# Kernel tuning notes

Hardware: AMD Instinct MI355X
Metric: run time of the kernel (lower is better)

The kernel has to match this reference:

```python
import jax, jax.numpy as jnp
import numpy as np

EMBED = 1024
ATTN = 1024
HEADS = 16
HEAD_DIM = ATTN // HEADS


def setup_inputs() -> dict:
    key = jax.random.key(0)
    ks = jax.random.split(key, 8)
    s = 1.0 / np.sqrt(EMBED)
    sa = 1.0 / np.sqrt(ATTN)
    return {
        "queries": jax.random.normal(ks[0], (4, 512, EMBED), jnp.float32),
        "context": jax.random.normal(ks[1], (4, 2048, EMBED), jnp.float32),
        "Wq": jax.random.normal(ks[2], (EMBED, ATTN), jnp.float32) * s,
        "bq": jnp.zeros((ATTN,), jnp.float32),
        "Wkv": jax.random.normal(ks[3], (EMBED, 2 * ATTN), jnp.float32) * s,
        "bkv": jnp.zeros((2 * ATTN,), jnp.float32),
        "Wo": jax.random.normal(ks[4], (ATTN, EMBED), jnp.float32) * sa,
        "bo": jnp.zeros((EMBED,), jnp.float32),
    }


def reference(queries, context, Wq, bq, Wkv, bkv, Wo, bo):
    B, Lq, _ = queries.shape
    Lk = context.shape[1]
    q = queries @ Wq + bq                      # [B, Lq, ATTN]
    kv = context @ Wkv + bkv                   # [B, Lk, 2*ATTN]
    k, v = jnp.split(kv, 2, axis=-1)
    q = q.reshape(B, Lq, HEADS, HEAD_DIM)
    k = k.reshape(B, Lk, HEADS, HEAD_DIM)
    v = v.reshape(B, Lk, HEADS, HEAD_DIM)
    scale = 1.0 / np.sqrt(HEAD_DIM)
    scores = jnp.einsum("bqhd,bkhd->bhqk", q, k) * scale
    attn = jax.nn.softmax(scores, axis=-1)
    x = jnp.einsum("bhqk,bkhd->bqhd", attn, v).reshape(B, Lq, ATTN)
    return x @ Wo + bo
```

## Files before the change

### kernel.cpp

```cpp
#include <hip/hip_runtime.h>
#include <hip/hip_bf16.h>
#include <stdint.h>

typedef unsigned short u16;
typedef __attribute__((ext_vector_type(8))) __bf16 bf16x8;
typedef __attribute__((ext_vector_type(2))) __bf16 bf16x2;
typedef __attribute__((ext_vector_type(4))) float f32x4;
typedef __attribute__((ext_vector_type(4))) u16 u16x4;
typedef __attribute__((ext_vector_type(4))) float f32x4v;

typedef __attribute__((address_space(1))) void gvoid_t;
typedef __attribute__((address_space(3))) void lvoid_t;

#define BAR()    asm volatile("s_barrier" ::: "memory")
#define WAITV0() asm volatile("s_waitcnt vmcnt(0)" ::: "memory")
#define WAITV2() asm volatile("s_waitcnt vmcnt(2)" ::: "memory")
#define WAITV4() asm volatile("s_waitcnt vmcnt(4)" ::: "memory")
#define WAITV8() asm volatile("s_waitcnt vmcnt(8)" ::: "memory")

__device__ inline u16 f2bf(float f) {
    uint32_t u = __float_as_uint(f);
    u += 0x7fff + ((u >> 16) & 1);
    return (u16)(u >> 16);
}

__device__ inline float bf2f(u16 v) {
    return __uint_as_float(((uint32_t)v) << 16);
}

__device__ inline void gll16(const void* g, void* l) {
    __builtin_amdgcn_global_load_lds((gvoid_t*)g, (lvoid_t*)l, 16, 0, 0);
}

__device__ inline f32x4 mfma16(bf16x8 a, bf16x8 b, f32x4 c) {
    return __builtin_amdgcn_mfma_f32_16x16x32_bf16(a, b, c, 0, 0, 0);
}

__device__ inline int vslot(int r) {
    int n = r >> 4;
    return ((n >> 1) << 5) + (((r >> 2) & 3) << 3) + ((n & 1) << 2) + (r & 3);
}

__global__ __launch_bounds__(256) void cast_bf16_kernel(
        const float* __restrict__ in, u16* __restrict__ out, int n4) {
    int i = blockIdx.x * 256 + threadIdx.x;
    if (i >= n4) return;
    f32x4v f = ((const f32x4v*)in)[i];
    u16x4 o;
    o[0] = f2bf(f[0]); o[1] = f2bf(f[1]); o[2] = f2bf(f[2]); o[3] = f2bf(f[3]);
    ((u16x4*)out)[i] = o;
}

__global__ __launch_bounds__(256) void trans_cast_kernel(
        const float* __restrict__ W, u16* __restrict__ WT, int K, int N) {
    __shared__ float t[32][33];
    int x = threadIdx.x;
    int y = threadIdx.y;
    int n0 = blockIdx.x * 32;
    int k0 = blockIdx.y * 32;
    for (int yy = y; yy < 32; yy += 8)
        t[yy][x] = W[(size_t)(k0 + yy) * N + n0 + x];
    __syncthreads();
    for (int yy = y; yy < 32; yy += 8)
        WT[(size_t)(n0 + yy) * K + k0 + x] = f2bf(t[x][yy]);
}

template <int MODE>
__global__ __launch_bounds__(512, 2) void gemm_bt(
        const u16* __restrict__ A, const u16* __restrict__ Bt,
        const float* __restrict__ bias, int M, int N, int K,
        float scale, void* __restrict__ out0) {
    __shared__ u16 lds[4][2][128 * 32];
    const int NT = K >> 5;
    const int tid = threadIdx.x;
    const int lane = tid & 63, wv = tid >> 6;
    const int c16 = lane & 15, g = lane >> 4;
    const int m0 = blockIdx.y * 128, n0 = blockIdx.x * 128;

    const int r0 = tid >> 2, cc0 = (tid & 3) ^ ((r0 >> 1) & 3);
    const size_t offA = (size_t)(m0 + r0) * K + cc0 * 8;
    const size_t offB = (size_t)(n0 + r0) * K + cc0 * 8;
    const int dstw = wv * 512;

    auto stage = [&](int t) {
        gll16(A + offA + t * 32, &lds[t & 3][0][0] + dstw);
        gll16(Bt + offB + t * 32, &lds[t & 3][1][0] + dstw);
    };

    const int wm = (wv >> 1) * 32, wn = (wv & 1) * 64;
    f32x4 acc[2][4] = {};

    auto compute = [&](int slot) {
        const u16* la = &lds[slot][0][0];
        const u16* lb = &lds[slot][1][0];
        bf16x8 af[2], bfr[4];
#pragma unroll
        for (int m = 0; m < 2; m++) {
            int row = wm + m * 16 + c16;
            af[m] = *(const bf16x8*)&la[row * 32 + (g ^ ((row >> 1) & 3)) * 8];
        }
#pragma unroll
        for (int n = 0; n < 4; n++) {
            int row = wn + n * 16 + c16;
            bfr[n] = *(const bf16x8*)&lb[row * 32 + (g ^ ((row >> 1) & 3)) * 8];
        }
#pragma unroll
        for (int m = 0; m < 2; m++)
#pragma unroll
            for (int n = 0; n < 4; n++)
                acc[m][n] = mfma16(af[m], bfr[n], acc[m][n]);
    };

    stage(0); stage(1); stage(2);

    for (int t = 0; t < NT - 2; ++t) {
        WAITV4();
        BAR();
        if (t + 3 < NT) stage(t + 3);
        compute(t & 3);
    }
    WAITV2(); BAR(); compute((NT - 2) & 3);
    WAITV0(); BAR(); compute((NT - 1) & 3);

#pragma unroll
    for (int n = 0; n < 4; n++) {
        int col = n0 + wn + n * 16 + c16;
        float bv = bias[col];
#pragma unroll
        for (int m = 0; m < 2; m++) {
            int rowb = m0 + wm + m * 16 + g * 4;
#pragma unroll
            for (int j = 0; j < 4; j++) {
                float v = (acc[m][n][j] + bv) * scale;
                int row = rowb + j;
                if (MODE == 0) {
                    ((u16*)out0)[(size_t)row * N + col] = f2bf(v);
                } else {
                    ((float*)out0)[(size_t)row * N + col] = v;
                }
            }
        }
    }
}

__global__ __launch_bounds__(512, 2) void gemm_kv_ring(
        const u16* __restrict__ A, const u16* __restrict__ Bt,
        const float* __restrict__ bias, u16* __restrict__ Kp,
        u16* __restrict__ VpT) {
    __shared__ u16 lds[4][2][256 * 32];
    const int K = 1024, NT = 32;
    const int tid = threadIdx.x;
    const int lane = tid & 63, wv = tid >> 6;
    const int c16 = lane & 15, g = lane >> 4;

    const int nwg = gridDim.x * gridDim.y;
    const int bid = blockIdx.y * gridDim.x + blockIdx.x;
    const int cpx = nwg >> 3;
    const int sw = (bid & 7) * cpx + (bid >> 3);
    const int bx = sw % gridDim.x, by = sw / gridDim.x;
    const int m0 = by * 256, n0 = bx * 256;

    const int isB = wv >> 2;
    const int rbase = (wv & 3) * 64;
    const u16* src = isB ? Bt : A;
    const int base0 = isB ? n0 : m0;
    size_t off[4];
    const u16* ldst[4];
#pragma unroll
    for (int i = 0; i < 4; i++) {
        int rl = rbase + i * 16 + (lane >> 2);
        int ch = (lane & 3) ^ ((rl >> 1) & 3);
        off[i] = (size_t)(base0 + rl) * K + ch * 8;
        ldst[i] = &lds[0][0][0] + ((size_t)isB * 256 * 32) + (size_t)(rbase + i * 16) * 32;
    }
    const size_t slotStride = 2 * 256 * 32;

    auto stage = [&](int t) {
        const u16* s0 = src + (size_t)t * 32;
        u16* d = (u16*)ldst[0] + (size_t)(t & 3) * slotStride;
        gll16(s0 + off[0], d);
        gll16(s0 + off[1], d + 16 * 32);
        gll16(s0 + off[2], d + 32 * 32);
        gll16(s0 + off[3], d + 48 * 32);
    };

    const int wm = wv >> 2;
    const int wn = wv & 3;
    f32x4 acc[8][4] = {};

    auto compute = [&](int slot) {
        const u16* la = &lds[slot][0][0];
        const u16* lb = &lds[slot][1][0];
        bf16x8 af[8], bfr[4];
#pragma unroll
        for (int m = 0; m < 8; m++) {
            int row = wm * 128 + m * 16 + c16;
            af[m] = *(const bf16x8*)&la[row * 32 + (g ^ ((row >> 1) & 3)) * 8];
        }
#pragma unroll
        for (int n = 0; n < 4; n++) {
            int row = wn * 64 + n * 16 + c16;
            bfr[n] = *(const bf16x8*)&lb[row * 32 + (g ^ ((row >> 1) & 3)) * 8];
        }
#pragma unroll
        for (int m = 0; m < 8; m++)
#pragma unroll
            for (int n = 0; n < 4; n++)
                acc[m][n] = mfma16(af[m], bfr[n], acc[m][n]);
    };

    stage(0); stage(1); stage(2);

    for (int t = 0; t < NT - 2; ++t) {
        WAITV8();
        BAR();
        if (t + 3 < NT) stage(t + 3);
        compute(t & 3);
    }
    WAITV4(); BAR(); compute((NT - 2) & 3);
    WAITV0(); BAR(); compute((NT - 1) & 3);

    const bool isV = (n0 >= 1024);
#pragma unroll
    for (int n = 0; n < 4; n++) {
        int col = n0 + wn * 64 + n * 16 + c16;
        float bv = bias[col];
#pragma unroll
        for (int m = 0; m < 8; m++) {
            int rowb = m0 + wm * 128 + m * 16 + g * 4;
            if (isV) {
                u16x4 pk;
#pragma unroll
                for (int j = 0; j < 4; j++) pk[j] = f2bf(acc[m][n][j] + bv);
                int vcol = (rowb & ~63) + vslot(rowb & 63);
                *(u16x4*)&VpT[(size_t)(col - 1024) * 8192 + vcol] = pk;
            } else {
#pragma unroll
                for (int j = 0; j < 4; j++)
                    Kp[(size_t)(rowb + j) * 1024 + col] = f2bf(acc[m][n][j] + bv);
            }
        }
    }
}

__global__ __launch_bounds__(512, 4) void attn_split_kernel(
        const u16* __restrict__ Qp, const u16* __restrict__ Kp,
        const u16* __restrict__ VpT, u16* __restrict__ Opart,
        float* __restrict__ ml) {
    __shared__ u16 lKV[3][2][64 * 64];
    const int NT = 16;
    const int tid = threadIdx.x;
    const int lane = tid & 63, wv = tid >> 6;
    const int c16 = lane & 15, g = lane >> 4;
    const int bid = blockIdx.x;
    const int qblk = bid >> 7;
    const int low = bid & 127;
    const int h = low & 15, z = low >> 4;
    const int b = z >> 1, sp = z & 1;
    const int kvbase = sp * 1024;

    const int qrow = b * 512 + qblk * 128 + wv * 16 + c16;
    bf16x8 qf[2];
    qf[0] = *(const bf16x8*)(Qp + (size_t)qrow * 1024 + h * 64 + g * 8);
    qf[1] = *(const bf16x8*)(Qp + (size_t)qrow * 1024 + h * 64 + 32 + g * 8);

    f32x4 acc[4] = {};
    float m_s = -1e30f, l_s = 0.f;

    const int r0 = tid >> 3, c0 = (tid & 7) ^ (r0 & 7);
    const int dstw = wv * 512;

    auto stageKV = [&](int t) {
        int slot = t % 3;
        int kv0 = kvbase + t * 64;
        u16* dK = &lKV[slot][0][0];
        u16* dV = &lKV[slot][1][0];
        gll16(Kp + (size_t)(b * 2048 + kv0 + r0) * 1024 + h * 64 + c0 * 8, dK + dstw);
        gll16(VpT + (size_t)(h * 64 + r0) * 8192 + b * 2048 + kv0 + c0 * 8, dV + dstw);
    };

    stageKV(0); stageKV(1);
    for (int t = 0; t < NT; ++t) {
        if (t < NT - 2) { WAITV2(); } else { WAITV0(); }
        BAR();
        if (t + 2 < NT) stageKV(t + 2);

        const int slot = t % 3;
        const u16* lK = &lKV[slot][0][0];
        const u16* lV = &lKV[slot][1][0];

        f32x4 s[4];
#pragma unroll
        for (int n = 0; n < 4; n++) {
            s[n] = f32x4{0.f, 0.f, 0.f, 0.f};
            int key = n * 16 + c16;
#pragma unroll
            for (int kk = 0; kk < 2; kk++) {
                bf16x8 kf = *(const bf16x8*)&lK[key * 64 + (((kk * 4 + g) ^ (key & 7))) * 8];
                s[n] = mfma16(kf, qf[kk], s[n]);
            }
        }

        float mn0 = fmaxf(fmaxf(s[0][0], s[0][1]), fmaxf(s[0][2], s[0][3]));
        float mn1 = fmaxf(fmaxf(s[1][0], s[1][1]), fmaxf(s[1][2], s[1][3]));
        float mn2 = fmaxf(fmaxf(s[2][0], s[2][1]), fmaxf(s[2][2], s[2][3]));
        float mn3 = fmaxf(fmaxf(s[3][0], s[3][1]), fmaxf(s[3][2], s[3][3]));
        float mx = fmaxf(fmaxf(mn0, mn1), fmaxf(mn2, mn3));
        mx = fmaxf(mx, __shfl_xor(mx, 16));
        mx = fmaxf(mx, __shfl_xor(mx, 32));

        if (!__all(mx - m_s <= 8.0f)) {
            float mn = fmaxf(m_s, mx);
            float al = exp2f(m_s - mn);
            m_s = mn;
            l_s *= al;
            float alr[4];
#pragma unroll
            for (int j = 0; j < 4; j++) alr[j] = __shfl(al, g * 4 + j);
#pragma unroll
            for (int nd = 0; nd < 4; nd++)
#pragma unroll
                for (int j = 0; j < 4; j++) acc[nd][j] *= alr[j];
        }

        uint32_t r[4][2];
        float sums[4];
#pragma unroll
        for (int n = 0; n < 4; n++) {
            float p0 = exp2f(s[n][0] - m_s);
            float p1 = exp2f(s[n][1] - m_s);
            float p2 = exp2f(s[n][2] - m_s);
            float p3 = exp2f(s[n][3] - m_s);
            sums[n] = (p0 + p1) + (p2 + p3);
            union { bf16x2 h; uint32_t u; } ca, cb;
            ca.h[0] = (__bf16)p0; ca.h[1] = (__bf16)p1;
            cb.h[0] = (__bf16)p2; cb.h[1] = (__bf16)p3;
            r[n][0] = ca.u; r[n][1] = cb.u;
        }
        float sum = (sums[0] + sums[1]) + (sums[2] + sums[3]);
        sum += __shfl_xor(sum, 16);
        sum += __shfl_xor(sum, 32);
        l_s += sum;

#pragma unroll
        for (int kk2 = 0; kk2 < 2; kk2++) {
            union { bf16x8 v8; uint32_t u[4]; } pa;
            pa.u[0] = r[kk2 * 2][0];
            pa.u[1] = r[kk2 * 2][1];
            pa.u[2] = r[kk2 * 2 + 1][0];
            pa.u[3] = r[kk2 * 2 + 1][1];
#pragma unroll
            for (int nd = 0; nd < 4; nd++) {
                int d = nd * 16 + c16;
                bf16x8 vf = *(const bf16x8*)&lV[d * 64 + (((kk2 * 4 + g) ^ (d & 7))) * 8];
                acc[nd] = mfma16(pa.v8, vf, acc[nd]);
            }
        }
    }

#pragma unroll
    for (int j = 0; j < 4; j++) {
        int rowq = b * 512 + qblk * 128 + wv * 16 + g * 4 + j;
        size_t idx = (size_t)sp * 32768 + (size_t)rowq * 16 + h;
#pragma unroll
        for (int nd = 0; nd < 4; nd++)
            Opart[idx * 64 + nd * 16 + c16] = f2bf(acc[nd][j]);
    }
    if (g == 0) {
        int rowq = b * 512 + qblk * 128 + wv * 16 + c16;
        size_t idx = (size_t)sp * 32768 + (size_t)rowq * 16 + h;
        ml[idx * 2] = m_s;
        ml[idx * 2 + 1] = l_s;
    }
}

__global__ __launch_bounds__(256) void attn_combine_kernel(
        const u16* __restrict__ Opart, const float* __restrict__ ml,
        u16* __restrict__ X) {
    const int tid = threadIdx.x;
    const int r = blockIdx.x * 4 + (tid >> 6);
    const int d = tid & 63;
    float m0 = ml[(size_t)r * 2], l0 = ml[(size_t)r * 2 + 1];
    float m1 = ml[(size_t)(32768 + r) * 2], l1 = ml[(size_t)(32768 + r) * 2 + 1];
    float M = fmaxf(m0, m1);
    float a0 = exp2f(m0 - M), a1 = exp2f(m1 - M);
    float li = 1.f / (l0 * a0 + l1 * a1);
    float o0 = bf2f(Opart[(size_t)r * 64 + d]);
    float o1 = bf2f(Opart[(size_t)(32768 + r) * 64 + d]);
    float o = (o0 * a0 + o1 * a1) * li;
    int qrow = r >> 4, h = r & 15;
    X[(size_t)qrow * 1024 + h * 64 + d] = f2bf(o);
}

extern "C" void kernel_launch(void* const* d_in, const int* in_sizes, int n_in,
                              void* d_out, int out_size, void* d_ws, size_t ws_size,
                              hipStream_t stream) {
    const float* queries = (const float*)d_in[0];
    const float* context = (const float*)d_in[1];
    const float* Wq      = (const float*)d_in[2];
    const float* bq      = (const float*)d_in[3];
    const float* Wkv     = (const float*)d_in[4];
    const float* bkv     = (const float*)d_in[5];
    const float* Wo      = (const float*)d_in[6];
    const float* bo      = (const float*)d_in[7];

    char* ws = (char*)d_ws;
    u16* qb   = (u16*)(ws);
    u16* cb   = (u16*)(ws + (4ull  << 20));
    u16* WqT  = (u16*)(ws + (20ull << 20));
    u16* WkvT = (u16*)(ws + (22ull << 20));
    u16* WoT  = (u16*)(ws + (26ull << 20));
    u16* Qp   = (u16*)(ws + (28ull << 20));
    u16* Kp   = (u16*)(ws + (32ull << 20));
    u16* VpT  = (u16*)(ws + (48ull << 20));
    u16* X    = (u16*)(ws + (64ull << 20));
    float* ml    = (float*)qb;
    u16*   Opart = (u16*)cb;

    cast_bf16_kernel<<<dim3(2048), dim3(256), 0, stream>>>(queries, qb, 524288);
    cast_bf16_kernel<<<dim3(8192), dim3(256), 0, stream>>>(context, cb, 2097152);
    trans_cast_kernel<<<dim3(32, 32), dim3(32, 8), 0, stream>>>(Wq, WqT, 1024, 1024);
    trans_cast_kernel<<<dim3(64, 32), dim3(32, 8), 0, stream>>>(Wkv, WkvT, 1024, 2048);
    trans_cast_kernel<<<dim3(32, 32), dim3(32, 8), 0, stream>>>(Wo, WoT, 1024, 1024);

    gemm_bt<0><<<dim3(8, 16), dim3(512), 0, stream>>>(qb, WqT, bq, 2048, 1024, 1024,
                                                      0.18033688f, (void*)Qp);
    gemm_kv_ring<<<dim3(8, 32), dim3(512), 0, stream>>>(cb, WkvT, bkv, Kp, VpT);
    attn_split_kernel<<<dim3(512), dim3(512), 0, stream>>>(Qp, Kp, VpT, Opart, ml);
    attn_combine_kernel<<<dim3(8192), dim3(256), 0, stream>>>(Opart, ml, X);
    gemm_bt<2><<<dim3(8, 16), dim3(512), 0, stream>>>(X, WoT, bo, 2048, 1024, 1024,
                                                      1.0f, d_out);
}
```

Baseline: 131.6 us.

## Process two query subtiles per wave in attention and merge prep kernels

The attention kernel drops to 256 threads per block, and each wave now handles two 16-row query subtiles. Each K/V fragment read from LDS is reused for twice as many MFMAs, and each thread issues four staging loads per tile instead of two. Separately, the two input cast launches are fused into one, and the three weight transpose-cast launches are fused into one 3D grid, cutting launch count. Register pressure in the attention kernel roughly doubles for accumulators and scores, and the wait count changes to vmcnt(4).

```diff
diff --git a/kernel.cpp b/kernel.cpp
--- a/kernel.cpp
+++ b/kernel.cpp
@@ -41,21 +41,32 @@
     return ((n >> 1) << 5) + (((r >> 2) & 3) << 3) + ((n & 1) << 2) + (r & 3);
 }
 
-__global__ __launch_bounds__(256) void cast_bf16_kernel(
-        const float* __restrict__ in, u16* __restrict__ out, int n4) {
+__global__ __launch_bounds__(256) void prep_cast_kernel(
+        const float* __restrict__ q, const float* __restrict__ c,
+        u16* __restrict__ qb, u16* __restrict__ cb) {
     int i = blockIdx.x * 256 + threadIdx.x;
-    if (i >= n4) return;
-    f32x4v f = ((const f32x4v*)in)[i];
+    const float* src; u16* dst; int j;
+    if (i < 524288) { src = q; dst = qb; j = i; }
+    else            { src = c; dst = cb; j = i - 524288; }
+    f32x4v f = ((const f32x4v*)src)[j];
     u16x4 o;
     o[0] = f2bf(f[0]); o[1] = f2bf(f[1]); o[2] = f2bf(f[2]); o[3] = f2bf(f[3]);
-    ((u16x4*)out)[i] = o;
-}
-
-__global__ __launch_bounds__(256) void trans_cast_kernel(
-        const float* __restrict__ W, u16* __restrict__ WT, int K, int N) {
+    ((u16x4*)dst)[j] = o;
+}
+
+__global__ __launch_bounds__(256) void prep_trans_kernel(
+        const float* __restrict__ Wq, const float* __restrict__ Wkv,
+        const float* __restrict__ Wo, u16* __restrict__ WqT,
+        u16* __restrict__ WkvT, u16* __restrict__ WoT) {
+    const int zz = blockIdx.z;
+    const float* W = (zz == 0) ? Wq : (zz == 1) ? Wkv : Wo;
+    u16* WT = (zz == 0) ? WqT : (zz == 1) ? WkvT : WoT;
+    const int N = (zz == 1) ? 2048 : 1024;
+    const int K = 1024;
+    if (blockIdx.x * 32 >= N) return;
     __shared__ float t[32][33];
-    int x = threadIdx.x;
-    int y = threadIdx.y;
+    int x = threadIdx.x & 31;
+    int y = threadIdx.x >> 5;
     int n0 = blockIdx.x * 32;
     int k0 = blockIdx.y * 32;
     for (int yy = y; yy < 32; yy += 8)
@@ -243,7 +254,7 @@
     }
 }
 
-__global__ __launch_bounds__(512, 4) void attn_split_kernel(
+__global__ __launch_bounds__(256, 3) void attn_split_kernel(
         const u16* __restrict__ Qp, const u16* __restrict__ Kp,
         const u16* __restrict__ VpT, u16* __restrict__ Opart,
         float* __restrict__ ml) {
@@ -259,29 +270,35 @@
     const int b = z >> 1, sp = z & 1;
     const int kvbase = sp * 1024;
 
-    const int qrow = b * 512 + qblk * 128 + wv * 16 + c16;
-    bf16x8 qf[2];
-    qf[0] = *(const bf16x8*)(Qp + (size_t)qrow * 1024 + h * 64 + g * 8);
-    qf[1] = *(const bf16x8*)(Qp + (size_t)qrow * 1024 + h * 64 + 32 + g * 8);
-
-    f32x4 acc[4] = {};
-    float m_s = -1e30f, l_s = 0.f;
+    bf16x8 qf[2][2];
+#pragma unroll
+    for (int qs = 0; qs < 2; qs++) {
+        int qrow = b * 512 + qblk * 128 + qs * 64 + wv * 16 + c16;
+        qf[qs][0] = *(const bf16x8*)(Qp + (size_t)qrow * 1024 + h * 64 + g * 8);
+        qf[qs][1] = *(const bf16x8*)(Qp + (size_t)qrow * 1024 + h * 64 + 32 + g * 8);
+    }
+
+    f32x4 acc[2][4] = {};
+    float m_s[2] = {-1e30f, -1e30f}, l_s[2] = {0.f, 0.f};
 
     const int r0 = tid >> 3, c0 = (tid & 7) ^ (r0 & 7);
-    const int dstw = wv * 512;
+    const int r1 = 32 + r0,  c1 = (tid & 7) ^ (r1 & 7);
+    const int dst0 = wv * 512, dst1 = 2048 + wv * 512;
 
     auto stageKV = [&](int t) {
         int slot = t % 3;
         int kv0 = kvbase + t * 64;
         u16* dK = &lKV[slot][0][0];
         u16* dV = &lKV[slot][1][0];
-        gll16(Kp + (size_t)(b * 2048 + kv0 + r0) * 1024 + h * 64 + c0 * 8, dK + dstw);
-        gll16(VpT + (size_t)(h * 64 + r0) * 8192 + b * 2048 + kv0 + c0 * 8, dV + dstw);
+        gll16(Kp + (size_t)(b * 2048 + kv0 + r0) * 1024 + h * 64 + c0 * 8, dK + dst0);
+        gll16(Kp + (size_t)(b * 2048 + kv0 + r1) * 1024 + h * 64 + c1 * 8, dK + dst1);
+        gll16(VpT + (size_t)(h * 64 + r0) * 8192 + b * 2048 + kv0 + c0 * 8, dV + dst0);
+        gll16(VpT + (size_t)(h * 64 + r1) * 8192 + b * 2048 + kv0 + c1 * 8, dV + dst1);
     };
 
     stageKV(0); stageKV(1);
     for (int t = 0; t < NT; ++t) {
-        if (t < NT - 2) { WAITV2(); } else { WAITV0(); }
+        if (t < NT - 1) { WAITV4(); } else { WAITV0(); }
         BAR();
         if (t + 2 < NT) stageKV(t + 2);
 
@@ -289,88 +306,100 @@
         const u16* lK = &lKV[slot][0][0];
         const u16* lV = &lKV[slot][1][0];
 
-        f32x4 s[4];
+        f32x4 s[2][4];
 #pragma unroll
         for (int n = 0; n < 4; n++) {
-            s[n] = f32x4{0.f, 0.f, 0.f, 0.f};
+            s[0][n] = f32x4{0.f, 0.f, 0.f, 0.f};
+            s[1][n] = f32x4{0.f, 0.f, 0.f, 0.f};
+        }
+#pragma unroll
+        for (int n = 0; n < 4; n++) {
             int key = n * 16 + c16;
 #pragma unroll
             for (int kk = 0; kk < 2; kk++) {
                 bf16x8 kf = *(const bf16x8*)&lK[key * 64 + (((kk * 4 + g) ^ (key & 7))) * 8];
-                s[n] = mfma16(kf, qf[kk], s[n]);
-            }
-        }
-
-        float mn0 = fmaxf(fmaxf(s[0][0], s[0][1]), fmaxf(s[0][2], s[0][3]));
-        float mn1 = fmaxf(fmaxf(s[1][0], s[1][1]), fmaxf(s[1][2], s[1][3]));
-        float mn2 = fmaxf(fmaxf(s[2][0], s[2][1]), fmaxf(s[2][2], s[2][3]));
-        float mn3 = fmaxf(fmaxf(s[3][0], s[3][1]), fmaxf(s[3][2], s[3][3]));
-        float mx = fmaxf(fmaxf(mn0, mn1), fmaxf(mn2, mn3));
-        mx = fmaxf(mx, __shfl_xor(mx, 16));
-        mx = fmaxf(mx, __shfl_xor(mx, 32));
-
-        if (!__all(mx - m_s <= 8.0f)) {
-            float mn = fmaxf(m_s, mx);
-            float al = exp2f(m_s - mn);
-            m_s = mn;
-            l_s *= al;
-            float alr[4];
-#pragma unroll
-            for (int j = 0; j < 4; j++) alr[j] = __shfl(al, g * 4 + j);
-#pragma unroll
-            for (int nd = 0; nd < 4; nd++)
-#pragma unroll
-                for (int j = 0; j < 4; j++) acc[nd][j] *= alr[j];
-        }
-
-        uint32_t r[4][2];
-        float sums[4];
-#pragma unroll
-        for (int n = 0; n < 4; n++) {
-            float p0 = exp2f(s[n][0] - m_s);
-            float p1 = exp2f(s[n][1] - m_s);
-            float p2 = exp2f(s[n][2] - m_s);
-            float p3 = exp2f(s[n][3] - m_s);
-            sums[n] = (p0 + p1) + (p2 + p3);
-            union { bf16x2 h; uint32_t u; } ca, cb;
-            ca.h[0] = (__bf16)p0; ca.h[1] = (__bf16)p1;
-            cb.h[0] = (__bf16)p2; cb.h[1] = (__bf16)p3;
-            r[n][0] = ca.u; r[n][1] = cb.u;
-        }
-        float sum = (sums[0] + sums[1]) + (sums[2] + sums[3]);
-        sum += __shfl_xor(sum, 16);
-        sum += __shfl_xor(sum, 32);
-        l_s += sum;
+                s[0][n] = mfma16(kf, qf[0][kk], s[0][n]);
+                s[1][n] = mfma16(kf, qf[1][kk], s[1][n]);
+            }
+        }
+
+        uint32_t r[2][4][2];
+#pragma unroll
+        for (int qs = 0; qs < 2; qs++) {
+            float mn0 = fmaxf(fmaxf(s[qs][0][0], s[qs][0][1]), fmaxf(s[qs][0][2], s[qs][0][3]));
+            float mn1 = fmaxf(fmaxf(s[qs][1][0], s[qs][1][1]), fmaxf(s[qs][1][2], s[qs][1][3]));
+            float mn2 = fmaxf(fmaxf(s[qs][2][0], s[qs][2][1]), fmaxf(s[qs][2][2], s[qs][2][3]));
+            float mn3 = fmaxf(fmaxf(s[qs][3][0], s[qs][3][1]), fmaxf(s[qs][3][2], s[qs][3][3]));
+            float mx = fmaxf(fmaxf(mn0, mn1), fmaxf(mn2, mn3));
+            mx = fmaxf(mx, __shfl_xor(mx, 16));
+            mx = fmaxf(mx, __shfl_xor(mx, 32));
+
+            if (!__all(mx - m_s[qs] <= 8.0f)) {
+                float mn = fmaxf(m_s[qs], mx);
+                float al = exp2f(m_s[qs] - mn);
+                m_s[qs] = mn;
+                l_s[qs] *= al;
+                float alr[4];
+#pragma unroll
+                for (int j = 0; j < 4; j++) alr[j] = __shfl(al, g * 4 + j);
+#pragma unroll
+                for (int nd = 0; nd < 4; nd++)
+#pragma unroll
+                    for (int j = 0; j < 4; j++) acc[qs][nd][j] *= alr[j];
+            }
+
+            float sums[4];
+#pragma unroll
+            for (int n = 0; n < 4; n++) {
+                float p0 = exp2f(s[qs][n][0] - m_s[qs]);
+                float p1 = exp2f(s[qs][n][1] - m_s[qs]);
+                float p2 = exp2f(s[qs][n][2] - m_s[qs]);
+                float p3 = exp2f(s[qs][n][3] - m_s[qs]);
+                sums[n] = (p0 + p1) + (p2 + p3);
+                union { bf16x2 h; uint32_t u; } ca, cb;
+                ca.h[0] = (__bf16)p0; ca.h[1] = (__bf16)p1;
+                cb.h[0] = (__bf16)p2; cb.h[1] = (__bf16)p3;
+                r[qs][n][0] = ca.u; r[qs][n][1] = cb.u;
+            }
+            float sum = (sums[0] + sums[1]) + (sums[2] + sums[3]);
+            sum += __shfl_xor(sum, 16);
+            sum += __shfl_xor(sum, 32);
+            l_s[qs] += sum;
+        }
 
 #pragma unroll
         for (int kk2 = 0; kk2 < 2; kk2++) {
-            union { bf16x8 v8; uint32_t u[4]; } pa;
-            pa.u[0] = r[kk2 * 2][0];
-            pa.u[1] = r[kk2 * 2][1];
-            pa.u[2] = r[kk2 * 2 + 1][0];
-            pa.u[3] = r[kk2 * 2 + 1][1];
+            union { bf16x8 v8; uint32_t u[4]; } pa0, pa1;
+            pa0.u[0] = r[0][kk2 * 2][0];     pa0.u[1] = r[0][kk2 * 2][1];
+            pa0.u[2] = r[0][kk2 * 2 + 1][0]; pa0.u[3] = r[0][kk2 * 2 + 1][1];
+            pa1.u[0] = r[1][kk2 * 2][0];     pa1.u[1] = r[1][kk2 * 2][1];
+            pa1.u[2] = r[1][kk2 * 2 + 1][0]; pa1.u[3] = r[1][kk2 * 2 + 1][1];
 #pragma unroll
             for (int nd = 0; nd < 4; nd++) {
                 int d = nd * 16 + c16;
                 bf16x8 vf = *(const bf16x8*)&lV[d * 64 + (((kk2 * 4 + g) ^ (d & 7))) * 8];
-                acc[nd] = mfma16(pa.v8, vf, acc[nd]);
-            }
-        }
-    }
-
-#pragma unroll
-    for (int j = 0; j < 4; j++) {
-        int rowq = b * 512 + qblk * 128 + wv * 16 + g * 4 + j;
-        size_t idx = (size_t)sp * 32768 + (size_t)rowq * 16 + h;
-#pragma unroll
-        for (int nd = 0; nd < 4; nd++)
-            Opart[idx * 64 + nd * 16 + c16] = f2bf(acc[nd][j]);
-    }
-    if (g == 0) {
-        int rowq = b * 512 + qblk * 128 + wv * 16 + c16;
-        size_t idx = (size_t)sp * 32768 + (size_t)rowq * 16 + h;
-        ml[idx * 2] = m_s;
-        ml[idx * 2 + 1] = l_s;
+                acc[0][nd] = mfma16(pa0.v8, vf, acc[0][nd]);
+                acc[1][nd] = mfma16(pa1.v8, vf, acc[1][nd]);
+            }
+        }
+    }
+
+#pragma unroll
+    for (int qs = 0; qs < 2; qs++) {
+#pragma unroll
+        for (int j = 0; j < 4; j++) {
+            int rowq = b * 512 + qblk * 128 + qs * 64 + wv * 16 + g * 4 + j;
+            size_t idx = (size_t)sp * 32768 + (size_t)rowq * 16 + h;
+#pragma unroll
+            for (int nd = 0; nd < 4; nd++)
+                Opart[idx * 64 + nd * 16 + c16] = f2bf(acc[qs][nd][j]);
+        }
+        if (g == 0) {
+            int rowq = b * 512 + qblk * 128 + qs * 64 + wv * 16 + c16;
+            size_t idx = (size_t)sp * 32768 + (size_t)rowq * 16 + h;
+            ml[idx * 2] = m_s[qs];
+            ml[idx * 2 + 1] = l_s[qs];
+        }
     }
 }
 
@@ -417,16 +446,14 @@
     float* ml    = (float*)qb;
     u16*   Opart = (u16*)cb;
 
-    cast_bf16_kernel<<<dim3(2048), dim3(256), 0, stream>>>(queries, qb, 524288);
-    cast_bf16_kernel<<<dim3(8192), dim3(256), 0, stream>>>(context, cb, 2097152);
-    trans_cast_kernel<<<dim3(32, 32), dim3(32, 8), 0, stream>>>(Wq, WqT, 1024, 1024);
-    trans_cast_kernel<<<dim3(64, 32), dim3(32, 8), 0, stream>>>(Wkv, WkvT, 1024, 2048);
-    trans_cast_kernel<<<dim3(32, 32), dim3(32, 8), 0, stream>>>(Wo, WoT, 1024, 1024);
+    prep_cast_kernel<<<dim3(10240), dim3(256), 0, stream>>>(queries, context, qb, cb);
+    prep_trans_kernel<<<dim3(64, 32, 3), dim3(256), 0, stream>>>(Wq, Wkv, Wo,
+                                                                 WqT, WkvT, WoT);
 
     gemm_bt<0><<<dim3(8, 16), dim3(512), 0, stream>>>(qb, WqT, bq, 2048, 1024, 1024,
                                                       0.18033688f, (void*)Qp);
     gemm_kv_ring<<<dim3(8, 32), dim3(512), 0, stream>>>(cb, WkvT, bkv, Kp, VpT);
-    attn_split_kernel<<<dim3(512), dim3(512), 0, stream>>>(Qp, Kp, VpT, Opart, ml);
+    attn_split_kernel<<<dim3(512), dim3(256), 0, stream>>>(Qp, Kp, VpT, Opart, ml);
     attn_combine_kernel<<<dim3(8192), dim3(256), 0, stream>>>(Opart, ml, X);
     gemm_bt<2><<<dim3(8, 16), dim3(512), 0, stream>>>(X, WoT, bo, 2048, 1024, 1024,
                                                       1.0f, d_out);
```

Result: faster. 125.9 us (-4.3%).
